# Performance work log

Measured on AMD Instinct MI355X. Metric: run time of the kernel, lower is better.

The kernel has to match this reference:

```python
import jax, jax.numpy as jnp
import numpy as np

D_MODEL, N_HEADS, D_FF = 512, 8, 2048
B, L = 2, 2048


def layer_norm(x, g, b, eps=1e-5):
    mu = jnp.mean(x, axis=-1, keepdims=True)
    var = jnp.mean(jnp.square(x - mu), axis=-1, keepdims=True)
    return (x - mu) * jax.lax.rsqrt(var + eps) * g + b


def setup_inputs() -> dict:
    key = jax.random.key(0)
    ks = jax.random.split(key, 16)
    s = 1.0 / np.sqrt(D_MODEL)
    sf = 1.0 / np.sqrt(D_FF)
    return {
        "x": jax.random.normal(ks[0], (B, L, D_MODEL), jnp.float32),
        "Wq": jax.random.normal(ks[1], (D_MODEL, D_MODEL), jnp.float32) * s,
        "bq": jnp.zeros((D_MODEL,), jnp.float32),
        "Wk": jax.random.normal(ks[2], (D_MODEL, D_MODEL), jnp.float32) * s,
        "bk": jnp.zeros((D_MODEL,), jnp.float32),
        "Wv": jax.random.normal(ks[3], (D_MODEL, D_MODEL), jnp.float32) * s,
        "bv": jnp.zeros((D_MODEL,), jnp.float32),
        "Wo": jax.random.normal(ks[4], (D_MODEL, D_MODEL), jnp.float32) * s,
        "bo": jnp.zeros((D_MODEL,), jnp.float32),
        "W1": jax.random.normal(ks[5], (D_FF, D_MODEL), jnp.float32) * s,   # conv1 k=1 -> linear
        "b1": jnp.zeros((D_FF,), jnp.float32),
        "W2": jax.random.normal(ks[6], (D_MODEL, D_FF), jnp.float32) * sf,  # conv2 k=1 -> linear
        "b2": jnp.zeros((D_MODEL,), jnp.float32),
        "g1": jnp.ones((D_MODEL,), jnp.float32),
        "be1": jnp.zeros((D_MODEL,), jnp.float32),
        "g2": jnp.ones((D_MODEL,), jnp.float32),
        "be2": jnp.zeros((D_MODEL,), jnp.float32),
    }


def reference(x, Wq, bq, Wk, bk, Wv, bv, Wo, bo, W1, b1, W2, b2, g1, be1, g2, be2):
    Bx, Lx, D = x.shape
    H = N_HEADS
    dk = D // H
    # projections -> [B, L, H, dk]
    q = (x @ Wq.T + bq).reshape(Bx, Lx, H, dk)
    k = (x @ Wk.T + bk).reshape(Bx, Lx, H, dk)
    v = (x @ Wv.T + bv).reshape(Bx, Lx, H, dk)
    scale = 1.0 / jnp.sqrt(jnp.asarray(dk, x.dtype))
    scores = jnp.einsum('blhd,bshd->bhls', q, k)  # full LxL score tensor (as in source)
    A = jax.nn.softmax(scale * scores, axis=-1)
    out = jnp.einsum('bhls,bshd->blhd', A, v).reshape(Bx, Lx, D)
    attn_out = out @ Wo.T + bo
    # residual + norm1 (dropout is identity in eval)
    x1 = layer_norm(x + attn_out, g1, be1)
    # FFN: conv1d with kernel_size=1 == pointwise linear
    y = jax.nn.relu(x1 @ W1.T + b1)
    y = y @ W2.T + b2
    return layer_norm(x1 + y, g2, be2)
```

## Files before the change

kernel.cpp:

```cpp
#include <hip/hip_runtime.h>
#include <hip/hip_bf16.h>
#include <cstddef>

#define SEQ 2048
#define DM  512
#define NH  8
#define DKH 64
#define DFF 2048
#define NB  2
#define MR  (NB*SEQ)

typedef __attribute__((ext_vector_type(8)))  short short8;
typedef __attribute__((ext_vector_type(4)))  float f32x4;
typedef __attribute__((ext_vector_type(16))) float f32x16;

#define AS1(p) ((const __attribute__((address_space(1))) void*)(p))
#define AS3(p) ((__attribute__((address_space(3))) void*)(p))

#define QSCALE 0.180336880f
#define SMAX 16.0f

__device__ inline unsigned cvtpk(float lo, float hi) {
  unsigned r;
  asm("v_cvt_pk_bf16_f32 %0, %1, %2" : "=v"(r) : "v"(lo), "v"(hi));
  return r;
}

__device__ inline void cvt8(const float* __restrict__ s, __hip_bfloat16* __restrict__ d) {
  float4 a = *reinterpret_cast<const float4*>(s);
  float4 b = *reinterpret_cast<const float4*>(s + 4);
  union { __hip_bfloat16 h[8]; short8 v; } u;
  u.h[0] = __float2bfloat16(a.x); u.h[1] = __float2bfloat16(a.y);
  u.h[2] = __float2bfloat16(a.z); u.h[3] = __float2bfloat16(a.w);
  u.h[4] = __float2bfloat16(b.x); u.h[5] = __float2bfloat16(b.y);
  u.h[6] = __float2bfloat16(b.z); u.h[7] = __float2bfloat16(b.w);
  *reinterpret_cast<short8*>(d) = u.v;
}

__global__ __launch_bounds__(256) void cvt_all(
    const float* __restrict__ x,
    const float* __restrict__ Wq, const float* __restrict__ Wk,
    const float* __restrict__ Wv, const float* __restrict__ Wo,
    const float* __restrict__ W1, const float* __restrict__ W2,
    const float* __restrict__ bq, const float* __restrict__ bk,
    const float* __restrict__ bv,
    __hip_bfloat16* __restrict__ xb,  __hip_bfloat16* __restrict__ wqkv,
    __hip_bfloat16* __restrict__ wob, __hip_bfloat16* __restrict__ w1b,
    __hip_bfloat16* __restrict__ w2b, float* __restrict__ bqkv)
{
  const int u = blockIdx.x * 256 + threadIdx.x;
  if (u < 262144) {
    cvt8(x + (size_t)u * 8, xb + (size_t)u * 8);
  } else if (u < 360448) {
    const int d = (u - 262144) * 8;
    const int n = d >> 9, k = d & 511;
    const float* src = (n < 512) ? (Wq + (size_t)n * 512 + k)
                     : (n < 1024) ? (Wk + (size_t)(n - 512) * 512 + k)
                                  : (Wv + (size_t)(n - 1024) * 512 + k);
    cvt8(src, wqkv + d);
  } else if (u < 393216) {
    const int d = (u - 360448) * 8; cvt8(Wo + d, wob + d);
  } else if (u < 524288) {
    const int d = (u - 393216) * 8; cvt8(W1 + d, w1b + d);
  } else if (u < 655360) {
    const int d = (u - 524288) * 8; cvt8(W2 + d, w2b + d);
  } else if (u < 655552) {
    const int d = (u - 655360) * 8;
    const float* src = (d < 512) ? (bq + d) : (d < 1024) ? (bk + d - 512) : (bv + d - 1024);
    *reinterpret_cast<float4*>(bqkv + d)     = *reinterpret_cast<const float4*>(src);
    *reinterpret_cast<float4*>(bqkv + d + 4) = *reinterpret_cast<const float4*>(src + 4);
  }
}

template<int OUT_BF16, int RELU, int WVT, int SPLITK>
__global__ __launch_bounds__(256) void gemm_bt(
    const __hip_bfloat16* __restrict__ A, const __hip_bfloat16* __restrict__ Bt,
    const float* __restrict__ bias, void* __restrict__ Cout, void* __restrict__ Cout1,
    __hip_bfloat16* __restrict__ qkbO, __hip_bfloat16* __restrict__ vtO,
    int M, int N, int K)
{
  __shared__ __align__(16) char lds[65536];
  const int t = threadIdx.x, lane = t & 63, w = t >> 6;

  const int nwg = gridDim.x * gridDim.y;
  int bid = blockIdx.y * gridDim.x + blockIdx.x;
  bid = (bid & 7) * (nwg >> 3) + (bid >> 3);
  const int bx = bid % gridDim.x, by = bid / gridDim.x;

  const int m0 = by * 128, n0 = bx * 128;
  const int wm = w >> 1, wn = w & 1;
  const int z = (SPLITK == 2) ? blockIdx.z : 0;
  const int Keff = (SPLITK == 2) ? (K >> 1) : K;
  const int koff = z * Keff;
  const int g = lane >> 4;

  const int r0   = t >> 3;
  const int kofs = ((lane & 7) ^ (r0 & 7)) * 8;
  const __hip_bfloat16* ap = A  + (size_t)(m0 + r0) * K + koff + kofs;
  const __hip_bfloat16* bp = Bt + (size_t)(n0 + r0) * K + koff + kofs;
  const int ldsoff = t * 16;

  const int fA = (wm * 64 + (lane & 15)) * 128;
  const int fB = (wn * 64 + (lane & 15)) * 128;
  const int sw = lane & 7;

  f32x4 acc[4][4] = {};
  const int nkt = Keff >> 6;

  auto STAGE = [&](int buf, int kt) {
    const size_t ko = (size_t)kt * 64;
    char* bb = lds + buf * 32768;
#pragma unroll
    for (int ii = 0; ii < 4; ++ii) {
      __builtin_amdgcn_global_load_lds(AS1(ap + (size_t)ii * 32 * K + ko), AS3(bb + ii * 4096 + ldsoff),         16, 0, 0);
      __builtin_amdgcn_global_load_lds(AS1(bp + (size_t)ii * 32 * K + ko), AS3(bb + 16384 + ii * 4096 + ldsoff), 16, 0, 0);
    }
  };
  auto COMPUTE = [&](const char* bb) {
    const char* Ab = bb;
    const char* Bb = bb + 16384;
#pragma unroll
    for (int kk = 0; kk < 2; ++kk) {
      const int cx = ((kk * 4 + g) ^ sw) * 16;
      short8 af[4], bf[4];
#pragma unroll
      for (int i = 0; i < 4; ++i) af[i] = *reinterpret_cast<const short8*>(Ab + fA + i * 2048 + cx);
#pragma unroll
      for (int j = 0; j < 4; ++j) bf[j] = *reinterpret_cast<const short8*>(Bb + fB + j * 2048 + cx);
      __builtin_amdgcn_s_setprio(1);
#pragma unroll
      for (int i = 0; i < 4; ++i)
#pragma unroll
        for (int j = 0; j < 4; ++j)
          acc[i][j] = __builtin_amdgcn_mfma_f32_16x16x32_bf16(af[i], bf[j], acc[i][j], 0, 0, 0);
      __builtin_amdgcn_s_setprio(0);
    }
  };

  STAGE(0, 0);
  __syncthreads();
  for (int kt = 0; kt < nkt; kt += 2) {
    STAGE(1, kt + 1 < nkt ? kt + 1 : kt);
    COMPUTE(lds);
    __syncthreads();
    STAGE(0, kt + 2 < nkt ? kt + 2 : kt);
    COMPUTE(lds + 32768);
    __syncthreads();
  }

  float bcol[4];
#pragma unroll
  for (int j = 0; j < 4; ++j)
    bcol[j] = (SPLITK == 2 && z) ? 0.f : bias[n0 + wn * 64 + j * 16 + (lane & 15)];

  if (WVT && n0 >= 1024) {
#pragma unroll
    for (int i = 0; i < 4; ++i) {
      const int r = m0 + wm * 64 + i * 16 + (g << 2);
      const int bb = r >> 11, s = r & 2047;
#pragma unroll
      for (int j = 0; j < 4; ++j) {
        const int hd = n0 + wn * 64 + j * 16 + (lane & 15) - 1024;
        union { __hip_bfloat16 h[4]; uint2 uu; } pk;
#pragma unroll
        for (int jj = 0; jj < 4; ++jj) pk.h[jj] = __float2bfloat16(acc[i][j][jj] + bcol[j]);
        *reinterpret_cast<uint2*>(vtO + ((size_t)(bb * 8 + (hd >> 6)) * 64 + (hd & 63)) * SEQ + s) = pk.uu;
      }
    }
    return;
  }

  const float qsc = (WVT && n0 < 512) ? QSCALE : 1.0f;
#pragma unroll
  for (int i = 0; i < 4; ++i) {
    const int row = m0 + wm * 64 + i * 16 + (g << 2);
#pragma unroll
    for (int j = 0; j < 4; ++j) {
      const int col = n0 + wn * 64 + j * 16 + (lane & 15);
#pragma unroll
      for (int jj = 0; jj < 4; ++jj) {
        float v = acc[i][j][jj] + bcol[j];
        if (RELU) v = fmaxf(v, 0.f);
        if (WVT)
          qkbO[(size_t)(row + jj) * 1024 + col] = __float2bfloat16(v * qsc);
        else if (OUT_BF16)
          ((__hip_bfloat16*)Cout)[(size_t)(row + jj) * N + col] = __float2bfloat16(v);
        else {
          float* dst = (float*)((SPLITK == 2 && z) ? Cout1 : Cout);
          dst[(size_t)(row + jj) * N + col] = v;
        }
      }
    }
  }
}

__global__ __launch_bounds__(256) void attn_mfma(
    const __hip_bfloat16* __restrict__ qkb, const __hip_bfloat16* __restrict__ vtb,
    __hip_bfloat16* __restrict__ po, float* __restrict__ pl)
{
  __shared__ __align__(16) char lds[32768];
  char* ks = lds;
  char* vT = lds + 16384;

  const int t = threadIdx.x, lane = t & 63, w = t >> 6;
  const int qt = blockIdx.x, bh = blockIdx.y, z = blockIdx.z;
  const int b = bh >> 3, h = bh & 7;
  const int ST0 = z * (SEQ / 4);
  const int NT = SEQ / 4 / 64;
  const int l31 = lane & 31, hi = lane >> 5;
  const int swz = (lane & 7) << 4;
  const int hi16 = hi * 16;

  const __hip_bfloat16* Qg = qkb + (size_t)b * SEQ * 1024 + h * DKH;
  const int qrow = qt * 128 + w * 32 + l31;
  short8 qf[4];
#pragma unroll
  for (int kc = 0; kc < 4; ++kc)
    qf[kc] = *reinterpret_cast<const short8*>(Qg + (size_t)qrow * 1024 + kc * 16 + hi * 8);

  const int srow = t >> 3;
  const int sofs = ((lane & 7) ^ (srow & 7)) * 8;
  const __hip_bfloat16* kbase = qkb + (size_t)(b * SEQ + ST0 + srow) * 1024 + 512 + h * DKH + sofs;
  const __hip_bfloat16* vbase = vtb + ((size_t)bh * 64 + srow) * SEQ + ST0 + sofs;
  const int ldso = t * 16;

  f32x16 o0 = {}, o1 = {};
  float l_ = 0.f;

  auto STAGE_K = [&](int buf, int st) {
    const size_t ko = (size_t)st * 64 * 1024;
    char* kd = ks + buf * 8192 + ldso;
    __builtin_amdgcn_global_load_lds(AS1(kbase + ko),                     AS3(kd),        16, 0, 0);
    __builtin_amdgcn_global_load_lds(AS1(kbase + ko + (size_t)32 * 1024), AS3(kd + 4096), 16, 0, 0);
  };
  auto STAGE_V = [&](int buf, int st) {
    const size_t vo = (size_t)st * 64;
    char* vd = vT + buf * 8192 + ldso;
    __builtin_amdgcn_global_load_lds(AS1(vbase + vo),                    AS3(vd),        16, 0, 0);
    __builtin_amdgcn_global_load_lds(AS1(vbase + vo + (size_t)32 * SEQ), AS3(vd + 4096), 16, 0, 0);
  };

  auto TILE = [&](const char* kb_, const char* vb_) {
#pragma unroll
    for (int half = 0; half < 2; ++half) {
      const int rbase = (half * 32 + l31) * 128;

      f32x16 acc = {};
      __builtin_amdgcn_s_setprio(1);
#pragma unroll
      for (int kc = 0; kc < 4; ++kc) {
        const int kbyte = (kc * 32 + hi16) ^ swz;
        const short8 ka = *reinterpret_cast<const short8*>(kb_ + rbase + kbyte);
        acc = __builtin_amdgcn_mfma_f32_32x32x16_bf16(ka, qf[kc], acc, 0, 0, 0);
      }
      __builtin_amdgcn_s_setprio(0);

      short8 pf[2];
      float ps = 0.f;
#pragma unroll
      for (int sc = 0; sc < 2; ++sc) {
        const int rb = sc * 8;
        float e0 = exp2f(acc[rb+0] - SMAX), e1 = exp2f(acc[rb+1] - SMAX);
        float e2 = exp2f(acc[rb+2] - SMAX), e3 = exp2f(acc[rb+3] - SMAX);
        float e4 = exp2f(acc[rb+4] - SMAX), e5 = exp2f(acc[rb+5] - SMAX);
        float e6 = exp2f(acc[rb+6] - SMAX), e7 = exp2f(acc[rb+7] - SMAX);
        ps += ((e0 + e1) + (e2 + e3)) + ((e4 + e5) + (e6 + e7));
        unsigned w0 = cvtpk(e0, e1), w1 = cvtpk(e2, e3);
        unsigned w2 = cvtpk(e4, e5), w3 = cvtpk(e6, e7);
        asm("v_permlane32_swap_b32 %0, %1" : "+v"(w0), "+v"(w2));
        asm("v_permlane32_swap_b32 %0, %1" : "+v"(w1), "+v"(w3));
        union { unsigned u[4]; short8 s8; } pu;
        pu.u[0] = w0; pu.u[1] = w1; pu.u[2] = w2; pu.u[3] = w3;
        pf[sc] = pu.s8;
      }
      ps += __shfl_xor(ps, 32);
      l_ += ps;

      __builtin_amdgcn_s_setprio(1);
#pragma unroll
      for (int kc = 0; kc < 2; ++kc) {
        const int sbyte = (half * 64 + kc * 32 + hi16) ^ swz;
        const short8 va0 = *reinterpret_cast<const short8*>(vb_ + l31 * 128 + sbyte);
        const short8 va1 = *reinterpret_cast<const short8*>(vb_ + (32 + l31) * 128 + sbyte);
        o0 = __builtin_amdgcn_mfma_f32_32x32x16_bf16(va0, pf[kc], o0, 0, 0, 0);
        o1 = __builtin_amdgcn_mfma_f32_32x32x16_bf16(va1, pf[kc], o1, 0, 0, 0);
      }
      __builtin_amdgcn_s_setprio(0);
    }
  };

  STAGE_K(0, 0);
  STAGE_V(0, 0);
  __syncthreads();

  for (int st = 0; st < NT; st += 2) {
    STAGE_V(1, st + 1);
    STAGE_K(1, st + 1);
    TILE(ks, vT);
    __syncthreads();
    const int nx = st + 2 < NT ? st + 2 : st + 1;
    STAGE_V(0, nx);
    STAGE_K(0, nx);
    TILE(ks + 8192, vT + 8192);
    __syncthreads();
  }

  {
    __hip_bfloat16* pz = po + (size_t)z * MR * DM;
    const size_t orow = (size_t)b * SEQ + qt * 128 + w * 32 + l31;
    __hip_bfloat16* dst = pz + orow * DM + h * DKH;
#pragma unroll
    for (int r = 0; r < 4; ++r) {
      uint2 u0, u1;
      u0.x = cvtpk(o0[4*r+0], o0[4*r+1]); u0.y = cvtpk(o0[4*r+2], o0[4*r+3]);
      u1.x = cvtpk(o1[4*r+0], o1[4*r+1]); u1.y = cvtpk(o1[4*r+2], o1[4*r+3]);
      *reinterpret_cast<uint2*>(dst + r * 8 + hi * 4)      = u0;
      *reinterpret_cast<uint2*>(dst + 32 + r * 8 + hi * 4) = u1;
    }
  }
  if (lane < 32) {
    const size_t idx = ((size_t)z * 16 + bh) * SEQ + qt * 128 + w * 32 + lane;
    pl[idx] = l_;
  }
}

__global__ __launch_bounds__(256) void attn_combine(
    const __hip_bfloat16* __restrict__ po, const float* __restrict__ pl,
    __hip_bfloat16* __restrict__ attnb)
{
  const int row  = blockIdx.x * 4 + (threadIdx.x >> 6);
  const int lane = threadIdx.x & 63;
  const int d0 = lane * 8, h = lane >> 3;
  const int b = row >> 11, qq = row & 2047;
  const size_t idx = ((size_t)b * 8 + h) * SEQ + qq;
  const size_t zs = (size_t)16 * SEQ;
  const float inv = 1.0f / (pl[idx] + pl[idx + zs] + pl[idx + 2*zs] + pl[idx + 3*zs]);
  float acc[8] = {};
  const size_t ro = (size_t)row * DM + d0;
#pragma unroll
  for (int zz = 0; zz < 4; ++zz) {
    short8 v = *reinterpret_cast<const short8*>(po + (size_t)zz * MR * DM + ro);
#pragma unroll
    for (int j = 0; j < 8; ++j) {
      const unsigned uu = ((unsigned)(unsigned short)v[j]) << 16;
      acc[j] += __builtin_bit_cast(float, uu);
    }
  }
  union { __hip_bfloat16 hh[8]; short8 s8; } u;
#pragma unroll
  for (int j = 0; j < 8; ++j) u.hh[j] = __float2bfloat16(acc[j] * inv);
  *reinterpret_cast<short8*>(attnb + ro) = u.s8;
}

template<int WB>
__global__ __launch_bounds__(256) void ln_res(
    const float* __restrict__ X, const float* __restrict__ Y0,
    const float* __restrict__ Y1,
    const float* __restrict__ g, const float* __restrict__ be,
    float* __restrict__ out, __hip_bfloat16* __restrict__ outb)
{
  const int row  = blockIdx.x * 4 + (threadIdx.x >> 6);
  const int lane = threadIdx.x & 63;
  const int c0   = lane * 8;
  const float* xr = X  + (size_t)row * DM;
  const float* y0 = Y0 + (size_t)row * DM;
  const float* y1 = Y1 + (size_t)row * DM;

  float v[8];
  float4 a0 = *reinterpret_cast<const float4*>(xr + c0);
  float4 a1 = *reinterpret_cast<const float4*>(xr + c0 + 4);
  float4 b0 = *reinterpret_cast<const float4*>(y0 + c0);
  float4 b1 = *reinterpret_cast<const float4*>(y0 + c0 + 4);
  float4 c0v= *reinterpret_cast<const float4*>(y1 + c0);
  float4 c1v= *reinterpret_cast<const float4*>(y1 + c0 + 4);
  v[0]=a0.x+b0.x+c0v.x; v[1]=a0.y+b0.y+c0v.y; v[2]=a0.z+b0.z+c0v.z; v[3]=a0.w+b0.w+c0v.w;
  v[4]=a1.x+b1.x+c1v.x; v[5]=a1.y+b1.y+c1v.y; v[6]=a1.z+b1.z+c1v.z; v[7]=a1.w+b1.w+c1v.w;

  float s = 0.f;
#pragma unroll
  for (int i = 0; i < 8; ++i) s += v[i];
#pragma unroll
  for (int off = 32; off >= 1; off >>= 1) s += __shfl_xor(s, off);
  const float mu = s * (1.0f/512.0f);

  float ss = 0.f;
#pragma unroll
  for (int i = 0; i < 8; ++i) { const float d = v[i] - mu; ss += d*d; }
#pragma unroll
  for (int off = 32; off >= 1; off >>= 1) ss += __shfl_xor(ss, off);
  const float rs = rsqrtf(ss * (1.0f/512.0f) + 1e-5f);

  float4 g0 = *reinterpret_cast<const float4*>(g  + c0);
  float4 g1 = *reinterpret_cast<const float4*>(g  + c0 + 4);
  float4 e0 = *reinterpret_cast<const float4*>(be + c0);
  float4 e1 = *reinterpret_cast<const float4*>(be + c0 + 4);
  float r[8];
  r[0]=(v[0]-mu)*rs*g0.x+e0.x; r[1]=(v[1]-mu)*rs*g0.y+e0.y;
  r[2]=(v[2]-mu)*rs*g0.z+e0.z; r[3]=(v[3]-mu)*rs*g0.w+e0.w;
  r[4]=(v[4]-mu)*rs*g1.x+e1.x; r[5]=(v[5]-mu)*rs*g1.y+e1.y;
  r[6]=(v[6]-mu)*rs*g1.z+e1.z; r[7]=(v[7]-mu)*rs*g1.w+e1.w;
  float4 o0, o1;
  o0.x=r[0]; o0.y=r[1]; o0.z=r[2]; o0.w=r[3];
  o1.x=r[4]; o1.y=r[5]; o1.z=r[6]; o1.w=r[7];
  *reinterpret_cast<float4*>(out + (size_t)row * DM + c0)     = o0;
  *reinterpret_cast<float4*>(out + (size_t)row * DM + c0 + 4) = o1;
  if (WB) {
    union { __hip_bfloat16 h[8]; short8 vv; } u;
#pragma unroll
    for (int i = 0; i < 8; ++i) u.h[i] = __float2bfloat16(r[i]);
    *reinterpret_cast<short8*>(outb + (size_t)row * DM + c0) = u.vv;
  }
}

extern "C" void kernel_launch(void* const* d_in, const int* in_sizes, int n_in,
                              void* d_out, int out_size, void* d_ws, size_t ws_size,
                              hipStream_t stream)
{
  const float* x   = (const float*)d_in[0];
  const float* Wq  = (const float*)d_in[1];
  const float* bq  = (const float*)d_in[2];
  const float* Wk  = (const float*)d_in[3];
  const float* bk  = (const float*)d_in[4];
  const float* Wv  = (const float*)d_in[5];
  const float* bv  = (const float*)d_in[6];
  const float* Wo  = (const float*)d_in[7];
  const float* bo  = (const float*)d_in[8];
  const float* W1  = (const float*)d_in[9];
  const float* b1  = (const float*)d_in[10];
  const float* W2  = (const float*)d_in[11];
  const float* b2  = (const float*)d_in[12];
  const float* g1  = (const float*)d_in[13];
  const float* be1 = (const float*)d_in[14];
  const float* g2  = (const float*)d_in[15];
  const float* be2 = (const float*)d_in[16];
  float* out = (float*)d_out;

  char* p = (char*)d_ws;
  __hip_bfloat16* xb    = (__hip_bfloat16*)p;  p += 4194304;
  __hip_bfloat16* wqkv  = (__hip_bfloat16*)p;  p += 1572864;
  __hip_bfloat16* wob   = (__hip_bfloat16*)p;  p += 524288;
  __hip_bfloat16* w1b   = (__hip_bfloat16*)p;  p += 2097152;
  __hip_bfloat16* w2b   = (__hip_bfloat16*)p;  p += 2097152;
  float*          bqkv  = (float*)p;           p += 8192;
  __hip_bfloat16* qkb   = (__hip_bfloat16*)p;  p += 8388608;
  __hip_bfloat16* vtb   = (__hip_bfloat16*)p;  p += 4194304;
  __hip_bfloat16* pob   = (__hip_bfloat16*)p;  p += 16777216;
  float*          pl    = (float*)p;           p += 524288;
  float*          oproj = (float*)p;           p += 8388608;
  __hip_bfloat16* x1b   = (__hip_bfloat16*)p;  p += 4194304;

  float*          x1    = (float*)qkb;
  __hip_bfloat16* attnb = (__hip_bfloat16*)vtb;
  float*          opa   = (float*)pob;
  __hip_bfloat16* f1b   = pob;
  float*          y2a   = (float*)d_ws;
  float*          y2b   = oproj;

  const dim3 blk(256);

  cvt_all<<<dim3(2561), blk, 0, stream>>>(x, Wq, Wk, Wv, Wo, W1, W2, bq, bk, bv,
                                          xb, wqkv, wob, w1b, w2b, bqkv);
  gemm_bt<1,0,1,0><<<dim3(12, 32), blk, 0, stream>>>(xb, wqkv, bqkv, nullptr, nullptr, qkb, vtb, MR, 1536, DM);
  attn_mfma   <<<dim3(SEQ/128, NB*NH, 4), blk, 0, stream>>>(qkb, vtb, pob, pl);
  attn_combine<<<dim3(MR/4), blk, 0, stream>>>(pob, pl, attnb);
  gemm_bt<0,0,0,2><<<dim3(4, 32, 2), blk, 0, stream>>>(attnb, wob, bo, opa, oproj, nullptr, nullptr, MR, DM, DM);
  ln_res<1><<<dim3(MR/4), blk, 0, stream>>>(x, opa, oproj, g1, be1, x1, x1b);
  gemm_bt<1,1,0,0><<<dim3(16, 32), blk, 0, stream>>>(x1b, w1b, b1, f1b, nullptr, nullptr, nullptr, MR, DFF, DM);
  gemm_bt<0,0,0,2><<<dim3(4, 32, 2), blk, 0, stream>>>(f1b, w2b, b2, y2a, y2b, nullptr, nullptr, MR, DM, DFF);
  ln_res<0><<<dim3(MR/4), blk, 0, stream>>>(x1, y2a, y2b, g2, be2, out, nullptr);
}
```

Measured before the change: 117.3 us.

## Swap MFMA operands for vectorized GEMM stores; use 512-thread attention with 2-way KV split

```diff
diff --git a/kernel.cpp b/kernel.cpp
--- a/kernel.cpp
+++ b/kernel.cpp
@@ -72,7 +72,7 @@
   }
 }
 
-template<int OUT_BF16, int RELU, int WVT, int SPLITK>
+template<int OUT_BF16, int RELU, int WVT, int SPLITK, int SWAPC>
 __global__ __launch_bounds__(256) void gemm_bt(
     const __hip_bfloat16* __restrict__ A, const __hip_bfloat16* __restrict__ Bt,
     const float* __restrict__ bias, void* __restrict__ Cout, void* __restrict__ Cout1,
@@ -132,7 +132,9 @@
       for (int i = 0; i < 4; ++i)
 #pragma unroll
         for (int j = 0; j < 4; ++j)
-          acc[i][j] = __builtin_amdgcn_mfma_f32_16x16x32_bf16(af[i], bf[j], acc[i][j], 0, 0, 0);
+          acc[i][j] = SWAPC
+            ? __builtin_amdgcn_mfma_f32_16x16x32_bf16(bf[j], af[i], acc[i][j], 0, 0, 0)
+            : __builtin_amdgcn_mfma_f32_16x16x32_bf16(af[i], bf[j], acc[i][j], 0, 0, 0);
       __builtin_amdgcn_s_setprio(0);
     }
   };
@@ -146,6 +148,35 @@
     STAGE(0, kt + 2 < nkt ? kt + 2 : kt);
     COMPUTE(lds + 32768);
     __syncthreads();
+  }
+
+  if (SWAPC) {
+#pragma unroll
+    for (int i = 0; i < 4; ++i) {
+      const int row = m0 + wm * 64 + i * 16 + (lane & 15);
+#pragma unroll
+      for (int j = 0; j < 4; ++j) {
+        const int colb = n0 + wn * 64 + j * 16 + (g << 2);
+        float4 bv;
+        if (SPLITK == 2 && z) { bv.x = bv.y = bv.z = bv.w = 0.f; }
+        else bv = *reinterpret_cast<const float4*>(&bias[colb]);
+        float v0 = acc[i][j][0] + bv.x, v1 = acc[i][j][1] + bv.y;
+        float v2 = acc[i][j][2] + bv.z, v3 = acc[i][j][3] + bv.w;
+        if (RELU) {
+          v0 = fmaxf(v0, 0.f); v1 = fmaxf(v1, 0.f);
+          v2 = fmaxf(v2, 0.f); v3 = fmaxf(v3, 0.f);
+        }
+        if (OUT_BF16) {
+          uint2 uu; uu.x = cvtpk(v0, v1); uu.y = cvtpk(v2, v3);
+          *reinterpret_cast<uint2*>((__hip_bfloat16*)Cout + (size_t)row * N + colb) = uu;
+        } else {
+          float* dst = (float*)((SPLITK == 2 && z) ? Cout1 : Cout);
+          float4 o; o.x = v0; o.y = v1; o.z = v2; o.w = v3;
+          *reinterpret_cast<float4*>(dst + (size_t)row * N + colb) = o;
+        }
+      }
+    }
+    return;
   }
 
   float bcol[4];
@@ -194,7 +225,7 @@
   }
 }
 
-__global__ __launch_bounds__(256) void attn_mfma(
+__global__ __launch_bounds__(512) void attn_mfma(
     const __hip_bfloat16* __restrict__ qkb, const __hip_bfloat16* __restrict__ vtb,
     __hip_bfloat16* __restrict__ po, float* __restrict__ pl)
 {
@@ -205,14 +236,14 @@
   const int t = threadIdx.x, lane = t & 63, w = t >> 6;
   const int qt = blockIdx.x, bh = blockIdx.y, z = blockIdx.z;
   const int b = bh >> 3, h = bh & 7;
-  const int ST0 = z * (SEQ / 4);
-  const int NT = SEQ / 4 / 64;
+  const int ST0 = z * (SEQ / 2);
+  const int NT = SEQ / 2 / 64;
   const int l31 = lane & 31, hi = lane >> 5;
   const int swz = (lane & 7) << 4;
   const int hi16 = hi * 16;
 
   const __hip_bfloat16* Qg = qkb + (size_t)b * SEQ * 1024 + h * DKH;
-  const int qrow = qt * 128 + w * 32 + l31;
+  const int qrow = qt * 256 + w * 32 + l31;
   short8 qf[4];
 #pragma unroll
   for (int kc = 0; kc < 4; ++kc)
@@ -228,16 +259,10 @@
   float l_ = 0.f;
 
   auto STAGE_K = [&](int buf, int st) {
-    const size_t ko = (size_t)st * 64 * 1024;
-    char* kd = ks + buf * 8192 + ldso;
-    __builtin_amdgcn_global_load_lds(AS1(kbase + ko),                     AS3(kd),        16, 0, 0);
-    __builtin_amdgcn_global_load_lds(AS1(kbase + ko + (size_t)32 * 1024), AS3(kd + 4096), 16, 0, 0);
+    __builtin_amdgcn_global_load_lds(AS1(kbase + (size_t)st * 64 * 1024), AS3(ks + buf * 8192 + ldso), 16, 0, 0);
   };
   auto STAGE_V = [&](int buf, int st) {
-    const size_t vo = (size_t)st * 64;
-    char* vd = vT + buf * 8192 + ldso;
-    __builtin_amdgcn_global_load_lds(AS1(vbase + vo),                    AS3(vd),        16, 0, 0);
-    __builtin_amdgcn_global_load_lds(AS1(vbase + vo + (size_t)32 * SEQ), AS3(vd + 4096), 16, 0, 0);
+    __builtin_amdgcn_global_load_lds(AS1(vbase + (size_t)st * 64),        AS3(vT + buf * 8192 + ldso), 16, 0, 0);
   };
 
   auto TILE = [&](const char* kb_, const char* vb_) {
@@ -307,7 +332,7 @@
 
   {
     __hip_bfloat16* pz = po + (size_t)z * MR * DM;
-    const size_t orow = (size_t)b * SEQ + qt * 128 + w * 32 + l31;
+    const size_t orow = (size_t)b * SEQ + qt * 256 + w * 32 + l31;
     __hip_bfloat16* dst = pz + orow * DM + h * DKH;
 #pragma unroll
     for (int r = 0; r < 4; ++r) {
@@ -319,7 +344,7 @@
     }
   }
   if (lane < 32) {
-    const size_t idx = ((size_t)z * 16 + bh) * SEQ + qt * 128 + w * 32 + lane;
+    const size_t idx = ((size_t)z * 16 + bh) * SEQ + qt * 256 + w * 32 + lane;
     pl[idx] = l_;
   }
 }
@@ -334,11 +359,11 @@
   const int b = row >> 11, qq = row & 2047;
   const size_t idx = ((size_t)b * 8 + h) * SEQ + qq;
   const size_t zs = (size_t)16 * SEQ;
-  const float inv = 1.0f / (pl[idx] + pl[idx + zs] + pl[idx + 2*zs] + pl[idx + 3*zs]);
+  const float inv = 1.0f / (pl[idx] + pl[idx + zs]);
   float acc[8] = {};
   const size_t ro = (size_t)row * DM + d0;
 #pragma unroll
-  for (int zz = 0; zz < 4; ++zz) {
+  for (int zz = 0; zz < 2; ++zz) {
     short8 v = *reinterpret_cast<const short8*>(po + (size_t)zz * MR * DM + ro);
 #pragma unroll
     for (int j = 0; j < 8; ++j) {
@@ -460,12 +485,12 @@
 
   cvt_all<<<dim3(2561), blk, 0, stream>>>(x, Wq, Wk, Wv, Wo, W1, W2, bq, bk, bv,
                                           xb, wqkv, wob, w1b, w2b, bqkv);
-  gemm_bt<1,0,1,0><<<dim3(12, 32), blk, 0, stream>>>(xb, wqkv, bqkv, nullptr, nullptr, qkb, vtb, MR, 1536, DM);
-  attn_mfma   <<<dim3(SEQ/128, NB*NH, 4), blk, 0, stream>>>(qkb, vtb, pob, pl);
+  gemm_bt<1,0,1,0,0><<<dim3(12, 32), blk, 0, stream>>>(xb, wqkv, bqkv, nullptr, nullptr, qkb, vtb, MR, 1536, DM);
+  attn_mfma   <<<dim3(SEQ/256, NB*NH, 2), dim3(512), 0, stream>>>(qkb, vtb, pob, pl);
   attn_combine<<<dim3(MR/4), blk, 0, stream>>>(pob, pl, attnb);
-  gemm_bt<0,0,0,2><<<dim3(4, 32, 2), blk, 0, stream>>>(attnb, wob, bo, opa, oproj, nullptr, nullptr, MR, DM, DM);
+  gemm_bt<0,0,0,2,1><<<dim3(4, 32, 2), blk, 0, stream>>>(attnb, wob, bo, opa, oproj, nullptr, nullptr, MR, DM, DM);
   ln_res<1><<<dim3(MR/4), blk, 0, stream>>>(x, opa, oproj, g1, be1, x1, x1b);
-  gemm_bt<1,1,0,0><<<dim3(16, 32), blk, 0, stream>>>(x1b, w1b, b1, f1b, nullptr, nullptr, nullptr, MR, DFF, DM);
-  gemm_bt<0,0,0,2><<<dim3(4, 32, 2), blk, 0, stream>>>(f1b, w2b, b2, y2a, y2b, nullptr, nullptr, MR, DM, DFF);
+  gemm_bt<1,1,0,0,1><<<dim3(16, 32), blk, 0, stream>>>(x1b, w1b, b1, f1b, nullptr, nullptr, nullptr, MR, DFF, DM);
+  gemm_bt<0,0,0,2,1><<<dim3(4, 32, 2), blk, 0, stream>>>(f1b, w2b, b2, y2a, y2b, nullptr, nullptr, MR, DM, DFF);
   ln_res<0><<<dim3(MR/4), blk, 0, stream>>>(x1, y2a, y2b, g2, be2, out, nullptr);
 }
```

Result: slower. 120.2 us (+2.4%).
